# Performance work log

Hardware: AMD Instinct MI355X
Metric: run time of the kernel (lower is better)

The kernel has to match this reference:

```python
import jax, jax.numpy as jnp
import numpy as np

N, E, G = 50000, 1600000, 500
H, F, NG, L, OUT = 128, 128, 50, 6, 1
LOG2 = float(np.log(2.0))

def ssp(x):
    return jax.nn.softplus(x) - LOG2

def setup_inputs() -> dict:
    key = jax.random.key(0)
    ks = jax.random.split(key, 16)
    inp = {
        'z': jax.random.randint(ks[0], (N,), 0, 100),
        'pos': jax.random.normal(ks[1], (N, 3), jnp.float32) * 5.0,
        'batch': jnp.sort(jax.random.randint(ks[2], (N,), 0, G)),
        'edge_index': jax.random.randint(ks[3], (2, E), 0, N),
        # parameters
        'emb': jax.random.normal(ks[4], (100, H), jnp.float32) * 0.1,
        'dist_W': jax.random.normal(ks[5], (1, NG), jnp.float32) * 0.1,
        'dist_b': jnp.zeros((NG,), jnp.float32),
        'Wn': jax.random.normal(ks[6], (L, H, F), jnp.float32) * (1.0 / np.sqrt(H)),
        'We': jax.random.normal(ks[7], (L, NG, F), jnp.float32) * (1.0 / np.sqrt(NG)),
        'be': jnp.zeros((L, F), jnp.float32),
        'Wo': jax.random.normal(ks[8], (L, F, H), jnp.float32) * (1.0 / np.sqrt(F)),
        'bo': jnp.zeros((L, H), jnp.float32),
        'W1': jax.random.normal(ks[9], (H, H // 2), jnp.float32) * (1.0 / np.sqrt(H)),
        'b1': jnp.zeros((H // 2,), jnp.float32),
        'W2': jax.random.normal(ks[10], (H // 2, OUT), jnp.float32) * (1.0 / np.sqrt(H // 2)),
        'b2': jnp.zeros((OUT,), jnp.float32),
    }
    return inp

def reference(z, pos, batch, edge_index, emb, dist_W, dist_b, Wn, We, be, Wo, bo, W1, b1, W2, b2):
    row, col = edge_index[0], edge_index[1]
    # edge distances -> Linear(1, num_gaussians)
    dist = jnp.linalg.norm(pos[row] - pos[col], axis=-1)            # [E]
    e = dist[:, None] * dist_W[0][None, :] + dist_b                 # [E, NG]
    v = emb[z]                                                      # [N, H]
    # edge-conditioned message passing x num_layers
    for i in range(Wn.shape[0]):
        h = v @ Wn[i]                                               # [N, F]
        msg = h[col] * (e @ We[i] + be[i])                          # [E, F]
        agg = jax.ops.segment_sum(msg, row, num_segments=v.shape[0])
        v = ssp(agg @ Wo[i] + bo[i])                                # [N, H]
    # readout
    u = ssp(v @ W1 + b1) @ W2 + b2                                  # [N, OUT]
    return jax.ops.segment_sum(u, batch, num_segments=G)            # [G, OUT]
```

## Files before the change

kernel.cpp:

```cpp
#include <hip/hip_runtime.h>
#include <math.h>

#define HDIM 128
#define NGAUSS 50
#define NLAYER 6
#define TSTR 136
#define DINV (1.0f/512.0f)
#define NXCD 8
#define NSTRIPE 512

typedef unsigned short ushortT;
typedef __attribute__((ext_vector_type(8))) short bf16x8;
typedef __attribute__((ext_vector_type(4))) float f32x4;

static __device__ __forceinline__ float bf2f(unsigned short u){
  union { unsigned int i; float f; } x; x.i = ((unsigned int)u) << 16; return x.f;
}
static __device__ __forceinline__ unsigned short f2bf(float f){
  union { float f; unsigned int i; } x; x.f = f;
  unsigned int i = x.i;
  unsigned int r = (i + 0x7FFFu + ((i >> 16) & 1u)) >> 16;
  return (unsigned short)r;
}
static __device__ __forceinline__ float ssp(float x){
  return fmaxf(x, 0.0f) + __logf(1.0f + __expf(-fabsf(x))) - 0.69314718055994530942f;
}
static __device__ __forceinline__ f32x4 mfma4r(const bf16x8* a, const bf16x8* b){
  f32x4 d = {0.f, 0.f, 0.f, 0.f};
  d = __builtin_amdgcn_mfma_f32_16x16x32_bf16(a[0], b[0], d, 0, 0, 0);
  d = __builtin_amdgcn_mfma_f32_16x16x32_bf16(a[1], b[1], d, 0, 0, 0);
  d = __builtin_amdgcn_mfma_f32_16x16x32_bf16(a[2], b[2], d, 0, 0, 0);
  d = __builtin_amdgcn_mfma_f32_16x16x32_bf16(a[3], b[3], d, 0, 0, 0);
  return d;
}


__global__ __launch_bounds__(256)
void k_hist(const int* __restrict__ erow, int* __restrict__ hist,
            int E, int NB, int shift, int estripe){
  __shared__ int lh[512];
  int tid = threadIdx.x, w = blockIdx.x;
  for (int i = tid; i < NB; i += 256) lh[i] = 0;
  __syncthreads();
  int beg = w * estripe;
  int end = beg + estripe; if (end > E) end = E;
  for (int e = beg + tid; e < end; e += 256)
    atomicAdd(&lh[erow[e] >> shift], 1);
  __syncthreads();
  for (int i = tid; i < NB; i += 256) hist[w * 512 + i] = lh[i];
}

__global__ __launch_bounds__(256)
void k_colscan(int* __restrict__ hist, int* __restrict__ colTotal, int NB){
  __shared__ int sA[512], sB[512];
  int b = blockIdx.x, tid = threadIdx.x;
  sA[tid]       = hist[tid * 512 + b];
  sA[tid + 256] = hist[(tid + 256) * 512 + b];
  __syncthreads();
  int* pa = sA; int* pb = sB;
  for (int off = 1; off < 512; off <<= 1){
    for (int i = tid; i < 512; i += 256)
      pb[i] = pa[i] + (i >= off ? pa[i - off] : 0);
    __syncthreads();
    int* t = pa; pa = pb; pb = t;
  }
  int e0 = (tid == 0) ? 0 : pa[tid - 1];
  int e1 = pa[tid + 255];
  hist[tid * 512 + b]       = e0;
  hist[(tid + 256) * 512 + b] = e1;
  if (tid == 0) colTotal[b] = pa[511];
}

__global__ __launch_bounds__(256)
void k_bscan(const int* __restrict__ colTotal, int* __restrict__ bucketBase, int NB){
  __shared__ int sA[512], sB[512];
  int tid = threadIdx.x;
  for (int i = tid; i < 512; i += 256) sA[i] = (i < NB) ? colTotal[i] : 0;
  __syncthreads();
  int* pa = sA; int* pb = sB;
  for (int off = 1; off < 512; off <<= 1){
    for (int i = tid; i < 512; i += 256)
      pb[i] = pa[i] + (i >= off ? pa[i - off] : 0);
    __syncthreads();
    int* t = pa; pa = pb; pb = t;
  }
  for (int i = tid; i < NB; i += 256)
    bucketBase[i] = (i == 0) ? 0 : pa[i - 1];
  if (tid == 0) bucketBase[NB] = pa[NB - 1];
}

__global__ __launch_bounds__(256)
void k_scatter(const int* __restrict__ erow, const int* __restrict__ ecol,
               const float* __restrict__ pos, const int* __restrict__ hist,
               const int* __restrict__ bucketBase, uint2* __restrict__ stg,
               int E, int NB, int shift, int estripe){
  __shared__ int cur[512];
  int tid = threadIdx.x, w = blockIdx.x;
  for (int b = tid; b < NB; b += 256)
    cur[b] = bucketBase[b] + hist[w * 512 + b];
  __syncthreads();
  int beg = w * estripe;
  int end = beg + estripe; if (end > E) end = E;
  int mask = (1 << shift) - 1;
  for (int e = beg + tid; e < end; e += 256){
    int r = erow[e], c = ecol[e];
    float dx = pos[r*3+0] - pos[c*3+0];
    float dy = pos[r*3+1] - pos[c*3+1];
    float dz = pos[r*3+2] - pos[c*3+2];
    float d = sqrtf(dx*dx + dy*dy + dz*dz);
    int du = (int)(d * 512.0f + 0.5f);
    if (du > 65535) du = 65535;
    int p = atomicAdd(&cur[r >> shift], 1);
    uint2 t;
    t.x = ((unsigned int)c << 16) | (unsigned int)du;
    t.y = (unsigned int)(r & mask);
    stg[p] = t;
  }
}

__global__ __launch_bounds__(256)
void k_place(const uint2* __restrict__ stg, const int* __restrict__ bucketBase,
             int* __restrict__ offsets, unsigned int* __restrict__ csr,
             int N, int NB, int shift, int E){
  __shared__ int rc[1024];
  __shared__ int sA[1024], sB[1024];
  int b = blockIdx.x, tid = threadIdx.x;
  int R = 1 << shift;
  int r0 = b << shift;
  int s = bucketBase[b], e2 = bucketBase[b + 1];
  for (int i = tid; i < R; i += 256) rc[i] = 0;
  __syncthreads();
  for (int j = s + tid; j < e2; j += 256)
    atomicAdd(&rc[stg[j].y], 1);
  __syncthreads();
  for (int i = tid; i < R; i += 256) sA[i] = rc[i];
  __syncthreads();
  int* pa = sA; int* pb = sB;
  for (int off = 1; off < R; off <<= 1){
    for (int i = tid; i < R; i += 256)
      pb[i] = pa[i] + (i >= off ? pa[i - off] : 0);
    __syncthreads();
    int* t = pa; pa = pb; pb = t;
  }
  for (int i = tid; i < R; i += 256){
    int excl = (i == 0) ? 0 : pa[i - 1];
    rc[i] = excl;
    int r = r0 + i;
    if (r < N) offsets[r] = s + excl;
  }
  if (b == NB - 1 && tid == 0) offsets[N] = E;
  __syncthreads();
  for (int j = s + tid; j < e2; j += 256){
    uint2 t = stg[j];
    int slot = s + atomicAdd(&rc[t.y], 1);
    csr[slot] = t.x;
  }
}

__global__ void k_setup(const int* __restrict__ z, const float* __restrict__ emb,
                        ushortT* __restrict__ vhi,
                        const float* __restrict__ Wn, ushortT* __restrict__ WnT,
                        const float* __restrict__ Wo, ushortT* __restrict__ WoT,
                        const float* __restrict__ dW, const float* __restrict__ db,
                        const float* __restrict__ We, const float* __restrict__ be,
                        float* __restrict__ a, float* __restrict__ c,
                        const int* __restrict__ batch, int* __restrict__ groupOff,
                        const float* __restrict__ W1, ushortT* __restrict__ W1T,
                        int N, int G, int B1, int B2, int B4, int B5, int B7){
  int b = blockIdx.x;
  int tid = threadIdx.x;
  if (b < B1){
    int idx = b * 256 + tid;
    if (idx < N * HDIM){
      int n = idx >> 7, f = idx & 127;
      vhi[idx] = f2bf(emb[z[n] * HDIM + f]);
    }
    return;
  }
  b -= B1;
  if (b < B2){
    int idx = b * 256 + tid;
    if (idx < NLAYER * HDIM * HDIM){
      int mat = idx >> 14, rem = idx & 16383;
      int n = rem >> 7, k = rem & 127;
      WnT[idx] = f2bf(Wn[(mat << 14) + k * HDIM + n]);
    }
    return;
  }
  b -= B2;
  if (b < B2){
    int idx = b * 256 + tid;
    if (idx < NLAYER * HDIM * HDIM){
      int mat = idx >> 14, rem = idx & 16383;
      int n = rem >> 7, k = rem & 127;
      WoT[idx] = f2bf(Wo[(mat << 14) + k * HDIM + n]);
    }
    return;
  }
  b -= B2;
  if (b < B4){
    int idx = b * 256 + tid;
    if (idx < NLAYER * HDIM){
      int l = idx >> 7, f = idx & 127;
      float av = 0.f, cv = 0.f;
      for (int g = 0; g < NGAUSS; ++g){
        float we = We[(l * NGAUSS + g) * HDIM + f];
        av += dW[g] * we;
        cv += db[g] * we;
      }
      a[idx] = av;
      c[idx] = cv + be[idx];
    }
    return;
  }
  b -= B4;
  if (b < B5){
    int i = b * 256 + tid;
    if (i >= N) return;
    int bb = batch[i];
    if (i == 0){
      for (int g = 0; g <= bb; ++g) groupOff[g] = 0;
    } else {
      int pb = batch[i - 1];
      for (int g = pb + 1; g <= bb; ++g) groupOff[g] = i;
    }
    if (i == N - 1){
      for (int g = bb + 1; g <= G; ++g) groupOff[g] = N;
    }
    return;
  }
  b -= B5;
  if (b < B7){
    int idx = b * 256 + tid;
    if (idx < 64 * HDIM){
      int ncol = idx >> 7, k = idx & 127;
      W1T[idx] = f2bf(W1[k * 64 + ncol]);
    }
  }
}

__global__ __launch_bounds__(128, 2)
void k_gemm0(const ushortT* __restrict__ X, const ushortT* __restrict__ WT,
             ushortT* __restrict__ outHi, int N){
  int tid = threadIdx.x;
  int wave = tid >> 6, lane = tid & 63;
  int m = lane & 15, quad = lane >> 4;
  int ntiles = (N + 15) >> 4;
  int t0 = (blockIdx.x * 2 + wave) * 2;
  if (t0 >= ntiles) return;

  bf16x8 av[2][4];
  #pragma unroll
  for (int rt = 0; rt < 2; ++rt){
    int row = (t0 + rt) * 16 + m; if (row >= N) row = N - 1;
    #pragma unroll
    for (int kk = 0; kk < 4; ++kk)
      av[rt][kk] = *(const bf16x8*)(X + ((size_t)row << 7) + kk*32 + quad*8);
  }
  #pragma unroll
  for (int ct = 0; ct < 8; ++ct){
    int ncol = ct * 16 + m;
    const ushortT* bp = WT + ((size_t)ncol << 7) + quad*8;
    bf16x8 bb[4];
    #pragma unroll
    for (int kk = 0; kk < 4; ++kk) bb[kk] = *(const bf16x8*)(bp + kk*32);
    #pragma unroll
    for (int rt = 0; rt < 2; ++rt){
      f32x4 d = mfma4r(av[rt], bb);
      #pragma unroll
      for (int r = 0; r < 4; ++r){
        int orow = (t0 + rt) * 16 + quad*4 + r;
        if (orow < N) outHi[((size_t)orow << 7) + ncol] = f2bf(d[r]);
      }
    }
  }
}

__global__ __launch_bounds__(256, 8)
void k_agg2(const ushortT* __restrict__ h, const int* __restrict__ offsets,
            const unsigned int* __restrict__ cd, const float* __restrict__ a,
            const float* __restrict__ c, ushortT* __restrict__ aggHi,
            int N, int segNodes){
  int xcd = blockIdx.x & (NXCD - 1);
  int idx = blockIdx.x >> 3;
  int node = xcd * segNodes + idx * 4 + (threadIdx.x >> 6);
  if (node >= N || node >= (xcd + 1) * segNodes) return;
  int lane = threadIdx.x & 63;
  int half = lane >> 5;
  int fl = (lane & 31) * 4;
  float4 av = *(const float4*)(a + fl);
  float4 cv = *(const float4*)(c + fl);
  int s = offsets[node], e = offsets[node + 1];
  float acc0 = 0.f, acc1 = 0.f, acc2 = 0.f, acc3 = 0.f;
  int j = s;
  for (; j + 8 <= e; j += 8){
    unsigned int q[4]; uint2 p[4];
    #pragma unroll
    for (int i = 0; i < 4; ++i) q[i] = cd[j + 2*i + half];
    #pragma unroll
    for (int i = 0; i < 4; ++i)
      p[i] = *(const uint2*)(h + ((size_t)(q[i] >> 16) << 7) + fl);
    #pragma unroll
    for (int i = 0; i < 4; ++i){
      float dd = (float)(q[i] & 0xFFFFu) * DINV;
      acc0 = fmaf(bf2f((ushortT)p[i].x),         fmaf(dd, av.x, cv.x), acc0);
      acc1 = fmaf(bf2f((ushortT)(p[i].x >> 16)), fmaf(dd, av.y, cv.y), acc1);
      acc2 = fmaf(bf2f((ushortT)p[i].y),         fmaf(dd, av.z, cv.z), acc2);
      acc3 = fmaf(bf2f((ushortT)(p[i].y >> 16)), fmaf(dd, av.w, cv.w), acc3);
    }
  }
  for (; j < e; j += 2){
    int myj = j + half;
    if (myj < e){
      unsigned int q = cd[myj];
      uint2 p = *(const uint2*)(h + ((size_t)(q >> 16) << 7) + fl);
      float dd = (float)(q & 0xFFFFu) * DINV;
      acc0 = fmaf(bf2f((ushortT)p.x),         fmaf(dd, av.x, cv.x), acc0);
      acc1 = fmaf(bf2f((ushortT)(p.x >> 16)), fmaf(dd, av.y, cv.y), acc1);
      acc2 = fmaf(bf2f((ushortT)p.y),         fmaf(dd, av.z, cv.z), acc2);
      acc3 = fmaf(bf2f((ushortT)(p.y >> 16)), fmaf(dd, av.w, cv.w), acc3);
    }
  }
  acc0 += __shfl_down(acc0, 32, 64);
  acc1 += __shfl_down(acc1, 32, 64);
  acc2 += __shfl_down(acc2, 32, 64);
  acc3 += __shfl_down(acc3, 32, 64);
  if (half == 0){
    uint2 ph;
    ph.x = (unsigned int)f2bf(acc0) | ((unsigned int)f2bf(acc1) << 16);
    ph.y = (unsigned int)f2bf(acc2) | ((unsigned int)f2bf(acc3) << 16);
    *(uint2*)(aggHi + ((size_t)node << 7) + fl) = ph;
  }
}

__global__ __launch_bounds__(128, 2)
void k_fpair(const ushortT* __restrict__ agg, const ushortT* __restrict__ WoT,
             const float* __restrict__ bo, const ushortT* __restrict__ WnT,
             ushortT* __restrict__ outH, int N, int segTiles){
  __shared__ ushortT vt[2][32 * TSTR];
  int tid = threadIdx.x;
  int wave = tid >> 6, lane = tid & 63;
  int m = lane & 15, quad = lane >> 4;
  int ntiles = (N + 15) >> 4;
  int xcd = blockIdx.x & (NXCD - 1);
  int idx = blockIdx.x >> 3;
  int wjIdx = idx * 2 + wave;
  int segWJ = segTiles >> 1;
  if (wjIdx >= segWJ) return;
  int t0 = xcd * segTiles + wjIdx * 2;
  if (t0 >= ntiles) return;
  ushortT* vw = vt[wave];

  bf16x8 av[2][4];
  #pragma unroll
  for (int rt = 0; rt < 2; ++rt){
    int row = (t0 + rt) * 16 + m; if (row >= N) row = N - 1;
    #pragma unroll
    for (int kk = 0; kk < 4; ++kk)
      av[rt][kk] = *(const bf16x8*)(agg + ((size_t)row << 7) + kk*32 + quad*8);
  }
  #pragma unroll
  for (int ct = 0; ct < 8; ++ct){
    int ncol = ct * 16 + m;
    const ushortT* bp = WoT + ((size_t)ncol << 7) + quad*8;
    bf16x8 bb[4];
    #pragma unroll
    for (int kk = 0; kk < 4; ++kk) bb[kk] = *(const bf16x8*)(bp + kk*32);
    float bbias = bo[ncol];
    #pragma unroll
    for (int rt = 0; rt < 2; ++rt){
      f32x4 d = mfma4r(av[rt], bb);
      #pragma unroll
      for (int r = 0; r < 4; ++r)
        vw[(rt*16 + quad*4 + r) * TSTR + ncol] = f2bf(ssp(d[r] + bbias));
    }
  }
  bf16x8 a2[2][4];
  #pragma unroll
  for (int rt = 0; rt < 2; ++rt){
    #pragma unroll
    for (int kk = 0; kk < 4; ++kk)
      a2[rt][kk] = *(const bf16x8*)(&vw[(rt*16 + m) * TSTR + kk*32 + quad*8]);
  }
  #pragma unroll
  for (int ct = 0; ct < 8; ++ct){
    int ncol = ct * 16 + m;
    const ushortT* bp = WnT + ((size_t)ncol << 7) + quad*8;
    bf16x8 bb[4];
    #pragma unroll
    for (int kk = 0; kk < 4; ++kk) bb[kk] = *(const bf16x8*)(bp + kk*32);
    #pragma unroll
    for (int rt = 0; rt < 2; ++rt){
      f32x4 d = mfma4r(a2[rt], bb);
      #pragma unroll
      for (int r = 0; r < 4; ++r){
        int orow = (t0 + rt) * 16 + quad*4 + r;
        if (orow < N) outH[((size_t)orow << 7) + ncol] = f2bf(d[r]);
      }
    }
  }
}

__global__ __launch_bounds__(128, 2)
void k_gfinal(const ushortT* __restrict__ agg, const ushortT* __restrict__ WoT,
              const float* __restrict__ bo, const ushortT* __restrict__ W1T,
              const float* __restrict__ b1, const float* __restrict__ W2,
              const float* __restrict__ b2, float* __restrict__ u,
              int N, int segTiles){
  __shared__ ushortT vt[2][32 * TSTR];
  int tid = threadIdx.x;
  int wave = tid >> 6, lane = tid & 63;
  int m = lane & 15, quad = lane >> 4;
  int ntiles = (N + 15) >> 4;
  int xcd = blockIdx.x & (NXCD - 1);
  int idx = blockIdx.x >> 3;
  int wjIdx = idx * 2 + wave;
  int segWJ = segTiles >> 1;
  if (wjIdx >= segWJ) return;
  int t0 = xcd * segTiles + wjIdx * 2;
  if (t0 >= ntiles) return;
  ushortT* vw = vt[wave];

  bf16x8 av[2][4];
  #pragma unroll
  for (int rt = 0; rt < 2; ++rt){
    int row = (t0 + rt) * 16 + m; if (row >= N) row = N - 1;
    #pragma unroll
    for (int kk = 0; kk < 4; ++kk)
      av[rt][kk] = *(const bf16x8*)(agg + ((size_t)row << 7) + kk*32 + quad*8);
  }
  #pragma unroll
  for (int ct = 0; ct < 8; ++ct){
    int ncol = ct * 16 + m;
    const ushortT* bp = WoT + ((size_t)ncol << 7) + quad*8;
    bf16x8 bb[4];
    #pragma unroll
    for (int kk = 0; kk < 4; ++kk) bb[kk] = *(const bf16x8*)(bp + kk*32);
    float bbias = bo[ncol];
    #pragma unroll
    for (int rt = 0; rt < 2; ++rt){
      f32x4 d = mfma4r(av[rt], bb);
      #pragma unroll
      for (int r = 0; r < 4; ++r)
        vw[(rt*16 + quad*4 + r) * TSTR + ncol] = f2bf(ssp(d[r] + bbias));
    }
  }
  bf16x8 a2[2][4];
  #pragma unroll
  for (int rt = 0; rt < 2; ++rt){
    #pragma unroll
    for (int kk = 0; kk < 4; ++kk)
      a2[rt][kk] = *(const bf16x8*)(&vw[(rt*16 + m) * TSTR + kk*32 + quad*8]);
  }
  float acc[2][4] = {{0.f,0.f,0.f,0.f},{0.f,0.f,0.f,0.f}};
  #pragma unroll
  for (int ct = 0; ct < 4; ++ct){
    int ncol = ct * 16 + m;
    const ushortT* bp = W1T + ((size_t)ncol << 7) + quad*8;
    bf16x8 bb[4];
    #pragma unroll
    for (int kk = 0; kk < 4; ++kk) bb[kk] = *(const bf16x8*)(bp + kk*32);
    float bb1 = b1[ncol];
    float w2  = W2[ncol];
    #pragma unroll
    for (int rt = 0; rt < 2; ++rt){
      f32x4 d = mfma4r(a2[rt], bb);
      #pragma unroll
      for (int r = 0; r < 4; ++r)
        acc[rt][r] += ssp(d[r] + bb1) * w2;
    }
  }
  float bb2 = b2[0];
  #pragma unroll
  for (int rt = 0; rt < 2; ++rt){
    #pragma unroll
    for (int r = 0; r < 4; ++r){
      float v = acc[rt][r];
      v += __shfl_xor(v, 1, 64);
      v += __shfl_xor(v, 2, 64);
      v += __shfl_xor(v, 4, 64);
      v += __shfl_xor(v, 8, 64);
      if (m == 0){
        int orow = (t0 + rt) * 16 + quad*4 + r;
        if (orow < N) u[orow] = v + bb2;
      }
    }
  }
}

__global__ void k_gsum(const float* __restrict__ u, const int* __restrict__ groupOff,
                       float* __restrict__ out, int G){
  int g = blockIdx.x * 4 + (threadIdx.x >> 6);
  if (g >= G) return;
  int lane = threadIdx.x & 63;
  int s = groupOff[g], e = groupOff[g + 1];
  float acc = 0.f;
  for (int j = s + lane; j < e; j += 64) acc += u[j];
  #pragma unroll
  for (int off = 32; off > 0; off >>= 1)
    acc += __shfl_down(acc, off, 64);
  if (lane == 0) out[g] = acc;
}

extern "C" void kernel_launch(void* const* d_in, const int* in_sizes, int n_in,
                              void* d_out, int out_size, void* d_ws, size_t ws_size,
                              hipStream_t stream){
  const int N = in_sizes[0];
  const int E = in_sizes[3] / 2;
  const int G = out_size;

  const int*   z     = (const int*)d_in[0];
  const float* pos   = (const float*)d_in[1];
  const int*   batch = (const int*)d_in[2];
  const int*   eidx  = (const int*)d_in[3];
  const int*   erow  = eidx;
  const int*   ecol  = eidx + E;
  const float* emb   = (const float*)d_in[4];
  const float* dW    = (const float*)d_in[5];
  const float* db    = (const float*)d_in[6];
  const float* Wn    = (const float*)d_in[7];
  const float* We    = (const float*)d_in[8];
  const float* be    = (const float*)d_in[9];
  const float* Wo    = (const float*)d_in[10];
  const float* bo    = (const float*)d_in[11];
  const float* W1    = (const float*)d_in[12];
  const float* b1    = (const float*)d_in[13];
  const float* W2    = (const float*)d_in[14];
  const float* b2    = (const float*)d_in[15];

  char* ws = (char*)d_ws;
  size_t off = 0;
  auto alloc = [&](size_t bytes) -> char* {
    char* p = ws + off;
    off = (off + bytes + 255) & ~(size_t)255;
    return p;
  };
  size_t hbytes = (size_t)N * HDIM * 2;
  size_t stgbytes = (size_t)E * 8;
  int*          offsets  = (int*)         alloc((size_t)(N + 1) * 4);
  unsigned int* csr      = (unsigned int*)alloc((size_t)E * 4);
  ushortT*      h0       = (ushortT*)     alloc(hbytes);
  ushortT*      h1       = (ushortT*)     alloc(hbytes);
  ushortT*      vhi      = (ushortT*)     alloc(hbytes);
  ushortT*      agghi    = (ushortT*)     alloc(hbytes);
  ushortT*      stgbuf   = (ushortT*)     alloc(stgbytes);
  ushortT*      WnT      = (ushortT*)     alloc((size_t)NLAYER * HDIM * HDIM * 2);
  ushortT*      WoT      = (ushortT*)     alloc((size_t)NLAYER * HDIM * HDIM * 2);
  ushortT*      W1T      = (ushortT*)     alloc((size_t)64 * HDIM * 2);
  float*        a        = (float*)       alloc((size_t)NLAYER * HDIM * 4);
  float*        c        = (float*)       alloc((size_t)NLAYER * HDIM * 4);
  float*        u        = (float*)       alloc((size_t)N * 4);
  int*          groupOff = (int*)         alloc((size_t)(G + 1) * 4);

  int*   hist       = (int*)h1;
  int*   colTotal   = hist + NSTRIPE * 512;
  int*   bucketBase = colTotal + 512;
  uint2* stg        = (uint2*)stgbuf;

  int shift = 7;
  while ((((N - 1) >> shift) + 1) > 512) ++shift;
  int NB = ((N - 1) >> shift) + 1;
  int estripe = (E + NSTRIPE - 1) / NSTRIPE;

  int B1 = (N * HDIM + 255) / 256;
  int B2 = (NLAYER * HDIM * HDIM + 255) / 256;
  int B4 = (NLAYER * HDIM + 255) / 256;
  int B5 = (N + 255) / 256;
  int B7 = (64 * HDIM + 255) / 256;
  k_setup<<<B1 + 2*B2 + B4 + B5 + B7, 256, 0, stream>>>(
      z, emb, vhi, Wn, WnT, Wo, WoT,
      dW, db, We, be, a, c, batch, groupOff, W1, W1T,
      N, G, B1, B2, B4, B5, B7);

  k_hist   <<<NSTRIPE, 256, 0, stream>>>(erow, hist, E, NB, shift, estripe);
  k_colscan<<<NB,      256, 0, stream>>>(hist, colTotal, NB);
  k_bscan  <<<1,       256, 0, stream>>>(colTotal, bucketBase, NB);
  k_scatter<<<NSTRIPE, 256, 0, stream>>>(erow, ecol, pos, hist, bucketBase,
                                         stg, E, NB, shift, estripe);
  k_place  <<<NB,      256, 0, stream>>>(stg, bucketBase, offsets, csr, N, NB, shift, E);

  int ntiles = (N + 15) >> 4;
  int segTiles = (((ntiles + NXCD - 1) / NXCD) + 1) & ~1;
  int segNodes = segTiles * 16;
  int segWJ = segTiles >> 1;
  int aggGrid  = NXCD * ((segNodes + 3) / 4);
  int gGrid    = NXCD * ((segWJ + 1) / 2);
  int nwj = (ntiles + 1) / 2;
  int pairGrid = (nwj + 1) / 2;
  k_gemm0<<<pairGrid, 128, 0, stream>>>(vhi, WnT, h0, N);

  for (int l = 0; l < NLAYER; ++l){
    size_t wo = (size_t)l * HDIM * HDIM;
    const ushortT* hin  = (l & 1) ? h1 : h0;
    ushortT*       hout = (l & 1) ? h0 : h1;
    k_agg2<<<aggGrid, 256, 0, stream>>>(hin, offsets, csr,
                                        a + l * HDIM, c + l * HDIM, agghi, N, segNodes);
    if (l < NLAYER - 1){
      size_t wn = (size_t)(l + 1) * HDIM * HDIM;
      k_fpair<<<gGrid, 128, 0, stream>>>(agghi, WoT + wo, bo + (size_t)l * HDIM,
                                         WnT + wn, hout, N, segTiles);
    } else {
      k_gfinal<<<gGrid, 128, 0, stream>>>(agghi, WoT + wo, bo + (size_t)l * HDIM,
                                          W1T, b1, W2, b2, u, N, segTiles);
    }
  }
  k_gsum<<<(G + 3) / 4, 256, 0, stream>>>(u, groupOff, (float*)d_out, G);
}
```

Measured before the change: 600.2 us.

## Restructure edge aggregation with 16-byte gathers and factored distance coefficients

The edge aggregation kernel now has each wave process four edges at once, with 16 lanes per edge each loading 8 bf16 features as a 16-byte vector instead of 8 bytes. The per-edge filter (d*a + c) is factored out, so the loop accumulates only sum(h) and sum(h*d), and a and c are applied once per node at the end. Edge records are read with nontemporal loads. This removes per-edge FMAs and issues fewer, wider gathers, at the cost of more accumulator registers and an extra shuffle-reduction stage.

```diff
diff --git a/kernel.cpp b/kernel.cpp
--- a/kernel.cpp
+++ b/kernel.cpp
@@ -15,6 +15,9 @@
 
 static __device__ __forceinline__ float bf2f(unsigned short u){
   union { unsigned int i; float f; } x; x.i = ((unsigned int)u) << 16; return x.f;
+}
+static __device__ __forceinline__ float bitsf(unsigned int i){
+  union { unsigned int i; float f; } x; x.i = i; return x.f;
 }
 static __device__ __forceinline__ unsigned short f2bf(float f){
   union { float f; unsigned int i; } x; x.f = f;
@@ -276,6 +279,22 @@
   }
 }
 
+#define AGG_PROC(P, DD) do { \
+    unsigned int w_; float lo_, hi_; \
+    w_ = (P).x; lo_ = bitsf(w_ << 16); hi_ = bitsf(w_ & 0xFFFF0000u); \
+    s1[0] = fmaf(lo_, (DD), s1[0]); s0[0] += lo_; \
+    s1[1] = fmaf(hi_, (DD), s1[1]); s0[1] += hi_; \
+    w_ = (P).y; lo_ = bitsf(w_ << 16); hi_ = bitsf(w_ & 0xFFFF0000u); \
+    s1[2] = fmaf(lo_, (DD), s1[2]); s0[2] += lo_; \
+    s1[3] = fmaf(hi_, (DD), s1[3]); s0[3] += hi_; \
+    w_ = (P).z; lo_ = bitsf(w_ << 16); hi_ = bitsf(w_ & 0xFFFF0000u); \
+    s1[4] = fmaf(lo_, (DD), s1[4]); s0[4] += lo_; \
+    s1[5] = fmaf(hi_, (DD), s1[5]); s0[5] += hi_; \
+    w_ = (P).w; lo_ = bitsf(w_ << 16); hi_ = bitsf(w_ & 0xFFFF0000u); \
+    s1[6] = fmaf(lo_, (DD), s1[6]); s0[6] += lo_; \
+    s1[7] = fmaf(hi_, (DD), s1[7]); s0[7] += hi_; \
+  } while(0)
+
 __global__ __launch_bounds__(256, 8)
 void k_agg2(const ushortT* __restrict__ h, const int* __restrict__ offsets,
             const unsigned int* __restrict__ cd, const float* __restrict__ a,
@@ -286,50 +305,56 @@
   int node = xcd * segNodes + idx * 4 + (threadIdx.x >> 6);
   if (node >= N || node >= (xcd + 1) * segNodes) return;
   int lane = threadIdx.x & 63;
-  int half = lane >> 5;
-  int fl = (lane & 31) * 4;
-  float4 av = *(const float4*)(a + fl);
-  float4 cv = *(const float4*)(c + fl);
+  int quarter = lane >> 4;
+  int fl = (lane & 15) * 8;
   int s = offsets[node], e = offsets[node + 1];
-  float acc0 = 0.f, acc1 = 0.f, acc2 = 0.f, acc3 = 0.f;
+  float s0[8] = {0.f,0.f,0.f,0.f,0.f,0.f,0.f,0.f};
+  float s1[8] = {0.f,0.f,0.f,0.f,0.f,0.f,0.f,0.f};
   int j = s;
   for (; j + 8 <= e; j += 8){
-    unsigned int q[4]; uint2 p[4];
-    #pragma unroll
-    for (int i = 0; i < 4; ++i) q[i] = cd[j + 2*i + half];
-    #pragma unroll
-    for (int i = 0; i < 4; ++i)
-      p[i] = *(const uint2*)(h + ((size_t)(q[i] >> 16) << 7) + fl);
-    #pragma unroll
-    for (int i = 0; i < 4; ++i){
-      float dd = (float)(q[i] & 0xFFFFu) * DINV;
-      acc0 = fmaf(bf2f((ushortT)p[i].x),         fmaf(dd, av.x, cv.x), acc0);
-      acc1 = fmaf(bf2f((ushortT)(p[i].x >> 16)), fmaf(dd, av.y, cv.y), acc1);
-      acc2 = fmaf(bf2f((ushortT)p[i].y),         fmaf(dd, av.z, cv.z), acc2);
-      acc3 = fmaf(bf2f((ushortT)(p[i].y >> 16)), fmaf(dd, av.w, cv.w), acc3);
-    }
-  }
-  for (; j < e; j += 2){
-    int myj = j + half;
+    unsigned int q0 = __builtin_nontemporal_load(cd + j + quarter);
+    unsigned int q1 = __builtin_nontemporal_load(cd + j + 4 + quarter);
+    uint4 p0 = *(const uint4*)(h + ((size_t)(q0 >> 16) << 7) + fl);
+    uint4 p1 = *(const uint4*)(h + ((size_t)(q1 >> 16) << 7) + fl);
+    float d0 = (float)(q0 & 0xFFFFu) * DINV;
+    float d1 = (float)(q1 & 0xFFFFu) * DINV;
+    AGG_PROC(p0, d0);
+    AGG_PROC(p1, d1);
+  }
+  for (; j < e; j += 4){
+    int myj = j + quarter;
     if (myj < e){
-      unsigned int q = cd[myj];
-      uint2 p = *(const uint2*)(h + ((size_t)(q >> 16) << 7) + fl);
+      unsigned int q = __builtin_nontemporal_load(cd + myj);
+      uint4 p = *(const uint4*)(h + ((size_t)(q >> 16) << 7) + fl);
       float dd = (float)(q & 0xFFFFu) * DINV;
-      acc0 = fmaf(bf2f((ushortT)p.x),         fmaf(dd, av.x, cv.x), acc0);
-      acc1 = fmaf(bf2f((ushortT)(p.x >> 16)), fmaf(dd, av.y, cv.y), acc1);
-      acc2 = fmaf(bf2f((ushortT)p.y),         fmaf(dd, av.z, cv.z), acc2);
-      acc3 = fmaf(bf2f((ushortT)(p.y >> 16)), fmaf(dd, av.w, cv.w), acc3);
-    }
-  }
-  acc0 += __shfl_down(acc0, 32, 64);
-  acc1 += __shfl_down(acc1, 32, 64);
-  acc2 += __shfl_down(acc2, 32, 64);
-  acc3 += __shfl_down(acc3, 32, 64);
-  if (half == 0){
-    uint2 ph;
-    ph.x = (unsigned int)f2bf(acc0) | ((unsigned int)f2bf(acc1) << 16);
-    ph.y = (unsigned int)f2bf(acc2) | ((unsigned int)f2bf(acc3) << 16);
-    *(uint2*)(aggHi + ((size_t)node << 7) + fl) = ph;
+      AGG_PROC(p, dd);
+    }
+  }
+  float4 av0 = *(const float4*)(a + fl);
+  float4 av1 = *(const float4*)(a + fl + 4);
+  float4 cv0 = *(const float4*)(c + fl);
+  float4 cv1 = *(const float4*)(c + fl + 4);
+  float r[8];
+  r[0] = av0.x * s1[0] + cv0.x * s0[0];
+  r[1] = av0.y * s1[1] + cv0.y * s0[1];
+  r[2] = av0.z * s1[2] + cv0.z * s0[2];
+  r[3] = av0.w * s1[3] + cv0.w * s0[3];
+  r[4] = av1.x * s1[4] + cv1.x * s0[4];
+  r[5] = av1.y * s1[5] + cv1.y * s0[5];
+  r[6] = av1.z * s1[6] + cv1.z * s0[6];
+  r[7] = av1.w * s1[7] + cv1.w * s0[7];
+  #pragma unroll
+  for (int k = 0; k < 8; ++k){
+    r[k] += __shfl_down(r[k], 32, 64);
+    r[k] += __shfl_down(r[k], 16, 64);
+  }
+  if (quarter == 0){
+    uint4 st;
+    st.x = (unsigned int)f2bf(r[0]) | ((unsigned int)f2bf(r[1]) << 16);
+    st.y = (unsigned int)f2bf(r[2]) | ((unsigned int)f2bf(r[3]) << 16);
+    st.z = (unsigned int)f2bf(r[4]) | ((unsigned int)f2bf(r[5]) << 16);
+    st.w = (unsigned int)f2bf(r[6]) | ((unsigned int)f2bf(r[7]) << 16);
+    *(uint4*)(aggHi + ((size_t)node << 7) + fl) = st;
   }
 }
 
```

Result: slower. 618.2 us (+3.0%).
